# Optimization experiments

Measured on AMD Instinct MI355X. Metric: run time of the kernel, lower is better.

Reference implementation:

```python
import jax, jax.numpy as jnp
import numpy as np

H = 2048          # hidden size
NH = 32           # query heads
NKV = 8           # kv heads
HD = H // NH      # head dim = 64
GROUPS = NH // NKV
S = 2048          # seq len
B = 1
SCALE = HD ** -0.5


def _rope_tables(seq, dim, base=10000.0):
    inv = 1.0 / (base ** (np.arange(0, dim, 2, dtype=np.float32) / dim))
    t = np.arange(seq, dtype=np.float32)
    freqs = np.outer(t, inv)                     # [S, dim/2]
    emb = np.concatenate([freqs, freqs], axis=-1)  # [S, dim]
    return jnp.asarray(np.cos(emb)), jnp.asarray(np.sin(emb))


def setup_inputs() -> dict:
    key = jax.random.key(0)
    ks = jax.random.split(key, 5)
    x = jax.random.normal(ks[0], (B, S, H), dtype=jnp.float32)
    wq = jax.random.normal(ks[1], (H, NH * HD), dtype=jnp.float32) * (H ** -0.5)
    wk = jax.random.normal(ks[2], (H, NKV * HD), dtype=jnp.float32) * (H ** -0.5)
    wv = jax.random.normal(ks[3], (H, NKV * HD), dtype=jnp.float32) * (H ** -0.5)
    wo = jax.random.normal(ks[4], (NH * HD, H), dtype=jnp.float32) * (H ** -0.5)
    cos, sin = _rope_tables(S, HD)
    mask = jnp.tril(jnp.ones((S, S), dtype=bool))[None, None]  # causal [1,1,S,S]
    return {"x": x, "wq": wq, "wk": wk, "wv": wv, "wo": wo,
            "cos": cos, "sin": sin, "mask": mask}


def _rotate_half(t):
    t1, t2 = jnp.split(t, 2, axis=-1)
    return jnp.concatenate([-t2, t1], axis=-1)


def reference(x, wq, wk, wv, wo, cos, sin, mask):
    b, s, _ = x.shape
    # projections
    q = (x @ wq).reshape(b, s, NH, HD).transpose(0, 2, 1, 3)    # [B,NH,S,HD]
    k = (x @ wk).reshape(b, s, NKV, HD).transpose(0, 2, 1, 3)   # [B,NKV,S,HD]
    v = (x @ wv).reshape(b, s, NKV, HD).transpose(0, 2, 1, 3)
    # RoPE (cos/sin broadcast over batch and heads)
    c = cos[None, None]; sn = sin[None, None]
    q = q * c + _rotate_half(q) * sn
    k = k * c + _rotate_half(k) * sn
    # GQA: repeat kv heads to match query heads
    k = jnp.repeat(k, GROUPS, axis=1)                           # [B,NH,S,HD]
    v = jnp.repeat(v, GROUPS, axis=1)
    # scores + causal mask + softmax (dropout p=0 -> identity in eval)
    scores = SCALE * jnp.einsum('bhqd,bhkd->bhqk', q, k)
    scores = jnp.where(mask, scores, -jnp.inf)
    attn = jax.nn.softmax(scores, axis=-1)
    out = jnp.einsum('bhqk,bhkd->bhqd', attn, v)
    out = out.transpose(0, 2, 1, 3).reshape(b, s, NH * HD)
    return out @ wo
```

## Files before the change

### kernel.cpp

```cpp
#include <hip/hip_runtime.h>

typedef unsigned short u16;
typedef unsigned u32;
typedef u16 u16x8 __attribute__((ext_vector_type(8)));
typedef u16 u16x4 __attribute__((ext_vector_type(4)));
typedef u32 u32x4 __attribute__((ext_vector_type(4)));
typedef __bf16 bf8 __attribute__((ext_vector_type(8)));
typedef float f32x4 __attribute__((ext_vector_type(4)));
typedef float f32x16 __attribute__((ext_vector_type(16)));

__device__ __forceinline__ u16 f2b(float f) {
  unsigned u = __float_as_uint(f);
  u += 0x7FFFu + ((u >> 16) & 1u);
  return (u16)(u >> 16);
}
__device__ __forceinline__ float b2f(u16 h) {
  return __uint_as_float(((unsigned)h) << 16);
}
__device__ __forceinline__ bf8 asbf8(u16x8 v) {
  return __builtin_bit_cast(bf8, v);
}
__device__ __forceinline__ void gll16(const u16* g, u16* l) {
  __builtin_amdgcn_global_load_lds(
      (const __attribute__((address_space(1))) unsigned*)(g),
      (__attribute__((address_space(3))) unsigned*)(l), 16, 0, 0);
}
__device__ __forceinline__ u32 cvtpk(float lo, float hi) {
  u32 r;
  asm("v_cvt_pk_bf16_f32 %0, %1, %2" : "=v"(r) : "v"(lo), "v"(hi));
  return r;
}
__device__ __forceinline__ void plswap(u32& a, u32& b) {
  asm("v_permlane32_swap_b32 %0, %1" : "+v"(a), "+v"(b));
}
__device__ __forceinline__ float ex2(float x) {
  return __builtin_amdgcn_exp2f(x);
}
#define MFMA32(A,B,C) __builtin_amdgcn_mfma_f32_32x32x16_bf16(A,B,C,0,0,0)


__global__ __launch_bounds__(256) void xconv(const float* __restrict__ x,
                                             u16* __restrict__ xb) {
  int i = (blockIdx.x * 256 + threadIdx.x) * 4;
  float4 v = *(const float4*)(x + i);
  u16x4 o;
  o[0] = f2b(v.x); o[1] = f2b(v.y); o[2] = f2b(v.z); o[3] = f2b(v.w);
  *(u16x4*)(xb + i) = o;
}

__global__ __launch_bounds__(256) void wtrans(const float* __restrict__ in,
                                              u16* __restrict__ out,
                                              int N, int K) {
  __shared__ float tile[32][33];
  int tx = threadIdx.x & 31, ty = threadIdx.x >> 5;
  int n0 = blockIdx.x * 32, k0 = blockIdx.y * 32;
#pragma unroll
  for (int yy = 0; yy < 32; yy += 8)
    tile[ty + yy][tx] = in[(size_t)(k0 + ty + yy) * N + n0 + tx];
  __syncthreads();
#pragma unroll
  for (int yy = 0; yy < 32; yy += 8)
    out[(size_t)(n0 + ty + yy) * K + k0 + tx] = f2b(tile[tx][ty + yy]);
}

__global__ __launch_bounds__(256) void reduce_qkv(u16* __restrict__ p0,
                                                  const u16* __restrict__ p1,
                                                  const float* __restrict__ cs,
                                                  const float* __restrict__ sn) {
  int idx = blockIdx.x * 256 + threadIdx.x;
  int s = idx / 384, c8 = (idx % 384) * 8;
  size_t base = (size_t)s * 3072 + c8;
  if (c8 < 2560) {
    int hc = c8 & 63;
    if (hc >= 32) return;
    u16x8 a0 = *(const u16x8*)(p0 + base);
    u16x8 a1 = *(const u16x8*)(p1 + base);
    u16x8 b0 = *(const u16x8*)(p0 + base + 32);
    u16x8 b1 = *(const u16x8*)(p1 + base + 32);
    u16x8 oa, ob;
#pragma unroll
    for (int e = 0; e < 8; ++e) {
      float va = b2f(a0[e]) + b2f(a1[e]);
      float vb = b2f(b0[e]) + b2f(b1[e]);
      float c1 = cs[s * 64 + hc + e],      s1 = sn[s * 64 + hc + e];
      float c2 = cs[s * 64 + hc + 32 + e], s2 = sn[s * 64 + hc + 32 + e];
      oa[e] = f2b(va * c1 - vb * s1);
      ob[e] = f2b(vb * c2 + va * s2);
    }
    *(u16x8*)(p0 + base)      = oa;
    *(u16x8*)(p0 + base + 32) = ob;
  } else {
    u16x8 a0 = *(const u16x8*)(p0 + base);
    u16x8 a1 = *(const u16x8*)(p1 + base);
    u16x8 o;
#pragma unroll
    for (int e = 0; e < 8; ++e) o[e] = f2b(b2f(a0[e]) + b2f(a1[e]));
    *(u16x8*)(p0 + base) = o;
  }
}

__global__ __launch_bounds__(256) void reduce_out(const u16* __restrict__ p0,
                                                  const u16* __restrict__ p1,
                                                  float* __restrict__ out) {
  int idx = blockIdx.x * 256 + threadIdx.x;
  size_t base = (size_t)idx * 8;
  u16x8 a0 = *(const u16x8*)(p0 + base);
  u16x8 a1 = *(const u16x8*)(p1 + base);
  float4 lo, hi;
  lo.x = b2f(a0[0]) + b2f(a1[0]); lo.y = b2f(a0[1]) + b2f(a1[1]);
  lo.z = b2f(a0[2]) + b2f(a1[2]); lo.w = b2f(a0[3]) + b2f(a1[3]);
  hi.x = b2f(a0[4]) + b2f(a1[4]); hi.y = b2f(a0[5]) + b2f(a1[5]);
  hi.z = b2f(a0[6]) + b2f(a1[6]); hi.w = b2f(a0[7]) + b2f(a1[7]);
  *(float4*)(out + base)     = lo;
  *(float4*)(out + base + 4) = hi;
}

__global__ __launch_bounds__(256) void kvtrans_f(const u16* __restrict__ qkv,
                                                 u16* __restrict__ Kf,
                                                 u16* __restrict__ Vf) {
  int bid = blockIdx.x;
  if (bid < 512) {
    int tid = bid * 256 + threadIdx.x;
    int s = tid >> 6, cc = tid & 63;
    int kh = cc >> 3, c = cc & 7;
    int j = c >> 1, hi = c & 1;
    int b = s >> 5, la = s & 31;
    u16x8 v = *(const u16x8*)(qkv + (size_t)s * 3072 + 2048 + cc * 8);
    *(u16x8*)(Kf + ((((size_t)(kh * 64 + b) * 4 + j) * 2 + hi) * 32 + la) * 8) = v;
  } else {
    int tid = (bid - 512) * 256 + threadIdx.x;
    int s = tid >> 6, cc = tid & 63;
    int kh = cc >> 3, c = cc & 7;
    int m = c >> 2, laB = (c & 3) * 8;
    int b = s >> 5, s5 = s & 31;
    int jj = s5 >> 4, hi = (s5 >> 3) & 1, e = s5 & 7;
    u16x8 v = *(const u16x8*)(qkv + (size_t)s * 3072 + 2560 + cc * 8);
    u16* dst = Vf + (((size_t)(kh * 64 + b) * 4 + m * 2 + jj) * 64 + hi * 32 + laB) * 8 + e;
#pragma unroll
    for (int i = 0; i < 8; ++i) dst[i * 8] = v[i];
  }
}


__global__ __launch_bounds__(256) void gemm_sk(const u16* __restrict__ A,
                                               const u16* __restrict__ Bt,
                                               u16* __restrict__ C0,
                                               u16* __restrict__ C1,
                                               int N, int Kfull, int KH) {
  __shared__ __align__(16) u16 As[128 * 64];
  __shared__ __align__(16) u16 Bs[128 * 64];
  const int t = threadIdx.x;
  const int lane = t & 63, wid = t >> 6;
  const int wm = (wid >> 1) * 64, wn = (wid & 1) * 64;
  const int la = lane & 15, lg = lane >> 4;
  const int m0 = blockIdx.y * 128, n0 = blockIdx.x * 128;
  const int kbeg = blockIdx.z * KH;
  u16* C = blockIdx.z ? C1 : C0;

  const int srow0 = wid * 32 + (lane >> 3);
  const int scolsw = (((lane & 7) ^ (lane >> 3))) * 8;
  const u16* Ap = A + (size_t)(m0 + srow0) * Kfull + kbeg + scolsw;
  const u16* Bp = Bt + (size_t)(n0 + srow0) * Kfull + kbeg + scolsw;
  u16* Adst = &As[wid * 2048];
  u16* Bdst = &Bs[wid * 2048];
  const size_t rstep8 = (size_t)8 * Kfull;

  f32x4 acc[4][4] = {};

  for (int k0 = 0; k0 < KH; k0 += 64) {
    __syncthreads();
#pragma unroll
    for (int cc = 0; cc < 4; ++cc)
      gll16(Ap + k0 + cc * rstep8, Adst + cc * 512);
#pragma unroll
    for (int cc = 0; cc < 4; ++cc)
      gll16(Bp + k0 + cc * rstep8, Bdst + cc * 512);
    __syncthreads();
#pragma unroll
    for (int kk = 0; kk < 2; ++kk) {
      bf8 af[4], bfr[4];
#pragma unroll
      for (int i = 0; i < 4; ++i) {
        const int row = wm + i * 16 + la;
        const int c8 = (kk * 4 + lg) ^ (row & 7);
        af[i] = asbf8(*(const u16x8*)(&As[row * 64 + c8 * 8]));
      }
#pragma unroll
      for (int j = 0; j < 4; ++j) {
        const int row = wn + j * 16 + la;
        const int c8 = (kk * 4 + lg) ^ (row & 7);
        bfr[j] = asbf8(*(const u16x8*)(&Bs[row * 64 + c8 * 8]));
      }
      __builtin_amdgcn_s_setprio(1);
#pragma unroll
      for (int i = 0; i < 4; ++i)
#pragma unroll
        for (int j = 0; j < 4; ++j)
          acc[i][j] = __builtin_amdgcn_mfma_f32_16x16x32_bf16(af[i], bfr[j],
                                                              acc[i][j], 0, 0, 0);
      __builtin_amdgcn_s_setprio(0);
    }
  }

#pragma unroll
  for (int i = 0; i < 4; ++i)
#pragma unroll
    for (int j = 0; j < 4; ++j)
#pragma unroll
      for (int r = 0; r < 4; ++r) {
        int row = m0 + wm + i * 16 + lg * 4 + r;
        int col = n0 + wn + j * 16 + la;
        C[(size_t)row * N + col] = f2b(acc[i][j][r]);
      }
}


#define STEPL(buf, bb) do {                                          \
    const u16* p_ = &smem[(((h2) << 1) | (buf)) * 4096 + lane8];     \
    bf8 K0 = asbf8(*(const u16x8*)(p_));                             \
    bf8 K1 = asbf8(*(const u16x8*)(p_ + 512));                       \
    bf8 K2 = asbf8(*(const u16x8*)(p_ + 1024));                      \
    bf8 K3 = asbf8(*(const u16x8*)(p_ + 1536));                      \
    bf8 V0 = asbf8(*(const u16x8*)(p_ + 2048));                      \
    bf8 V1 = asbf8(*(const u16x8*)(p_ + 2560));                      \
    bf8 V2 = asbf8(*(const u16x8*)(p_ + 3072));                      \
    bf8 V3 = asbf8(*(const u16x8*)(p_ + 3584));                      \
    f32x16 s = {};                                                   \
    __builtin_amdgcn_s_setprio(1);                                   \
    s = MFMA32(K0, qf0, s);                                          \
    s = MFMA32(K1, qf1, s);                                          \
    s = MFMA32(K2, qf2, s);                                          \
    s = MFMA32(K3, qf3, s);                                          \
    __builtin_amdgcn_s_setprio(0);                                   \
    if ((bb) == kmax) {                                              \
      _Pragma("unroll") for (int r = 0; r < 16; ++r) {               \
        int kvr = (bb) * 32 + (r & 3) + 8 * (r >> 2) + 4 * hi;       \
        if (kvr > q0w + la) s[r] = -1e30f;                           \
      }                                                              \
    }                                                                \
    _Pragma("unroll") for (int r = 0; r < 16; ++r)                   \
      s[r] = ex2(s[r] - 32.0f);                                      \
    float z0 = s[0] + s[1],   z1 = s[2] + s[3];                      \
    float z2 = s[4] + s[5],   z3 = s[6] + s[7];                      \
    float z4 = s[8] + s[9],   z5 = s[10] + s[11];                    \
    float z6 = s[12] + s[13], z7 = s[14] + s[15];                    \
    l_run += ((z0 + z1) + (z2 + z3)) + ((z4 + z5) + (z6 + z7));      \
    u32 c0 = cvtpk(s[0], s[1]),   c1 = cvtpk(s[2], s[3]);            \
    u32 c2 = cvtpk(s[4], s[5]),   c3 = cvtpk(s[6], s[7]);            \
    u32 c4 = cvtpk(s[8], s[9]),   c5 = cvtpk(s[10], s[11]);          \
    u32 c6 = cvtpk(s[12], s[13]), c7 = cvtpk(s[14], s[15]);          \
    plswap(c0, c2); plswap(c1, c3); plswap(c4, c6); plswap(c5, c7);  \
    u32x4 t0; t0[0] = c0; t0[1] = c1; t0[2] = c2; t0[3] = c3;        \
    u32x4 t1; t1[0] = c4; t1[1] = c5; t1[2] = c6; t1[3] = c7;        \
    bf8 pa0 = __builtin_bit_cast(bf8, t0);                           \
    bf8 pa1 = __builtin_bit_cast(bf8, t1);                           \
    __builtin_amdgcn_s_setprio(1);                                   \
    o0 = MFMA32(pa0, V0, o0);                                        \
    o0 = MFMA32(pa1, V1, o0);                                        \
    o1 = MFMA32(pa0, V2, o1);                                        \
    o1 = MFMA32(pa1, V3, o1);                                        \
    __builtin_amdgcn_s_setprio(0);                                   \
  } while (0)

#define STG(bb, buf) do {                                            \
    u16* d_ = &smem[((((h2) << 1) | (buf)) * 4096) + wq * 1024];     \
    const u16* kp_ = Kg + (size_t)(bb) * 2048 + wq * 1024 + lane8;   \
    const u16* vp_ = Vg + (size_t)(bb) * 2048 + wq * 1024 + lane8;   \
    gll16(kp_, d_);                                                  \
    gll16(kp_ + 512, d_ + 512);                                      \
    gll16(vp_, d_ + 2048);                                           \
    gll16(vp_ + 512, d_ + 2560);                                     \
  } while (0)

__global__ __launch_bounds__(256, 4) void attn_fwd(const u16* __restrict__ qkv,
                                                   const u16* __restrict__ Kf,
                                                   const u16* __restrict__ Vf,
                                                   u16* __restrict__ aout) {
  const int head = blockIdx.x;
  const int qt = 31 - (int)blockIdx.y;
  const int Q0 = qt * 64;
  const int Kb = qt * 2;
  const int nb = Kb + 2;
  const int ha = nb >> 1;
  const int kh = head >> 2;
  const int t = threadIdx.x;
  const int w = t >> 6, lane = t & 63;
  const int h2 = w >> 1;
  const int wq = w & 1;
  const int la = lane & 31;
  const int hi = lane >> 5;
  const int lane8 = lane * 8;
  const int q0w = Q0 + 32 * wq;
  const int kmax = Kb + wq;

  __shared__ __align__(16) u16 smem[16384];
  __shared__ float lM[4][32];

  bf8 qf0, qf1, qf2, qf3;
  {
    const u16* qp = qkv + (size_t)(q0w + la) * 3072 + head * 64 + hi * 8;
    const float SC = 0.125f * 1.44269504088896340736f;
#define QLOAD(dst, kk) do {                                          \
      u16x8 v = *(const u16x8*)(qp + (kk) * 16);                     \
      u16x8 sv;                                                      \
      _Pragma("unroll") for (int e = 0; e < 8; ++e)                  \
        sv[e] = f2b(b2f(v[e]) * SC);                                 \
      dst = asbf8(sv);                                               \
    } while (0)
    QLOAD(qf0, 0); QLOAD(qf1, 1); QLOAD(qf2, 2); QLOAD(qf3, 3);
#undef QLOAD
  }

  const u16* Kg = Kf + (size_t)kh * 131072;
  const u16* Vg = Vf + (size_t)kh * 131072;

  f32x16 o0 = {}, o1 = {};
  float l_run = 0.f;

  STG(h2 ? ha : 0, 0);
  __syncthreads();

  for (int i = 0; i < ha; ++i) {
    if (i + 1 < ha) STG(h2 ? (ha + i + 1) : (i + 1), (i + 1) & 1);
    const int bb = h2 ? (ha + i) : i;
    if (bb <= kmax) STEPL(i & 1, bb);
    __syncthreads();
  }

  {
    float lt = l_run + __shfl_xor(l_run, 32);
    if (lane < 32) lM[w][lane] = lt;
#pragma unroll
    for (int r = 0; r < 16; ++r) {
      int crow = (r & 3) + 8 * (r >> 2) + 4 * hi;
      smem[(w * 32 + crow) * 72 + la]      = f2b(o0[r]);
      smem[(w * 32 + crow) * 72 + la + 32] = f2b(o1[r]);
    }
  }
  __syncthreads();

#pragma unroll
  for (int it = 0; it < 2; ++it) {
    const int id = t + it * 256;
    const int q = id >> 3, d0 = (id & 7) * 8;
    const int wA = q >> 5, crow = q & 31;
    float inv = 1.0f / (lM[wA][crow] + lM[wA + 2][crow]);
    u16x8 a = *(const u16x8*)&smem[((wA)     * 32 + crow) * 72 + d0];
    u16x8 b = *(const u16x8*)&smem[((wA + 2) * 32 + crow) * 72 + d0];
    u16x8 outv;
#pragma unroll
    for (int j = 0; j < 8; ++j)
      outv[j] = f2b((b2f(a[j]) + b2f(b[j])) * inv);
    *(u16x8*)(aout + (size_t)(Q0 + q) * 2048 + head * 64 + d0) = outv;
  }
}


extern "C" void kernel_launch(void* const* d_in, const int* in_sizes, int n_in,
                              void* d_out, int out_size, void* d_ws, size_t ws_size,
                              hipStream_t stream) {
  (void)in_sizes; (void)n_in; (void)out_size; (void)ws_size;
  const float* x  = (const float*)d_in[0];
  const float* wq = (const float*)d_in[1];
  const float* wk = (const float*)d_in[2];
  const float* wv = (const float*)d_in[3];
  const float* wo = (const float*)d_in[4];
  const float* cs = (const float*)d_in[5];
  const float* sn = (const float*)d_in[6];

  u16* ws    = (u16*)d_ws;
  u16* xb    = ws;
  u16* wqkvT = ws + 4194304;
  u16* qkv   = ws + 10485760;
  u16* woT   = ws + 16777216;
  u16* ext   = ws + 20971520;
  u16* Kf    = wqkvT;
  u16* Vf    = wqkvT + 1048576;
  u16* aout  = xb;
  u16* op0   = qkv;
  u16* op1   = ext;

  xconv<<<4096, 256, 0, stream>>>(x, xb);
  wtrans<<<dim3(64, 64), 256, 0, stream>>>(wq, wqkvT, 2048, 2048);
  wtrans<<<dim3(16, 64), 256, 0, stream>>>(wk, wqkvT + (size_t)2048 * 2048, 512, 2048);
  wtrans<<<dim3(16, 64), 256, 0, stream>>>(wv, wqkvT + (size_t)2560 * 2048, 512, 2048);
  wtrans<<<dim3(64, 64), 256, 0, stream>>>(wo, woT, 2048, 2048);

  gemm_sk<<<dim3(24, 16, 2), 256, 0, stream>>>(xb, wqkvT, qkv, ext, 3072, 2048, 1024);
  reduce_qkv<<<3072, 256, 0, stream>>>(qkv, ext, cs, sn);
  kvtrans_f<<<1024, 256, 0, stream>>>(qkv, Kf, Vf);
  attn_fwd<<<dim3(32, 32), 256, 0, stream>>>(qkv, Kf, Vf, aout);
  gemm_sk<<<dim3(16, 16, 2), 256, 0, stream>>>(aout, woT, op0, op1, 2048, 2048, 1024);
  reduce_out<<<2048, 256, 0, stream>>>(op0, op1, (float*)d_out);
}
```

Measured before the change: 140.5 us.

## Fuse KV layout transform into reduce kernel and stage 64-key blocks in attention

The split-K reduction kernel now writes the RoPE'd K and the summed V straight into the fragment layouts the attention kernel consumes, so the separate kvtrans_f launch and its extra pass over K/V are gone. The attention kernel now stages 64-key blocks (two 32-key groups) per iteration with doubled shared memory, halving the number of barriers and loop steps. The larger LDS footprint lowers the occupancy hint from 4 to 2 blocks per CU, which risks less latency hiding. The V path now does scattered 2-byte stores from the reduce kernel.

```diff
diff --git a/kernel.cpp b/kernel.cpp
--- a/kernel.cpp
+++ b/kernel.cpp
@@ -65,6 +65,8 @@
 
 __global__ __launch_bounds__(256) void reduce_qkv(u16* __restrict__ p0,
                                                   const u16* __restrict__ p1,
+                                                  u16* __restrict__ Kf,
+                                                  u16* __restrict__ Vf,
                                                   const float* __restrict__ cs,
                                                   const float* __restrict__ sn) {
   int idx = blockIdx.x * 256 + threadIdx.x;
@@ -87,15 +89,31 @@
       oa[e] = f2b(va * c1 - vb * s1);
       ob[e] = f2b(vb * c2 + va * s2);
     }
-    *(u16x8*)(p0 + base)      = oa;
-    *(u16x8*)(p0 + base + 32) = ob;
+    if (c8 < 2048) {
+      *(u16x8*)(p0 + base)      = oa;
+      *(u16x8*)(p0 + base + 32) = ob;
+    } else {
+      int kh = (c8 - 2048) >> 6;
+      int d0 = hc;
+      int b = s >> 5, la = s & 31;
+      int j0 = d0 >> 4, hi0 = (d0 >> 3) & 1;
+      size_t f0 = ((((size_t)(kh * 64 + b) * 4 + j0) * 2 + hi0) * 32 + la) * 8;
+      size_t f1 = ((((size_t)(kh * 64 + b) * 4 + j0 + 2) * 2 + hi0) * 32 + la) * 8;
+      *(u16x8*)(Kf + f0) = oa;
+      *(u16x8*)(Kf + f1) = ob;
+    }
   } else {
     u16x8 a0 = *(const u16x8*)(p0 + base);
     u16x8 a1 = *(const u16x8*)(p1 + base);
-    u16x8 o;
-#pragma unroll
-    for (int e = 0; e < 8; ++e) o[e] = f2b(b2f(a0[e]) + b2f(a1[e]));
-    *(u16x8*)(p0 + base) = o;
+    int c = c8 - 2560;
+    int kh = c >> 6, d0 = c & 63;
+    int m = d0 >> 5, la0 = d0 & 31;
+    int b = s >> 5, s5 = s & 31;
+    int jj = s5 >> 4, hi = (s5 >> 3) & 1, e = s5 & 7;
+    u16* dst = Vf + (((size_t)(kh * 64 + b) * 4 + m * 2 + jj) * 64 + hi * 32 + la0) * 8 + e;
+#pragma unroll
+    for (int i = 0; i < 8; ++i)
+      dst[i * 8] = f2b(b2f(a0[i]) + b2f(a1[i]));
   }
 }
 
@@ -115,32 +133,6 @@
   *(float4*)(out + base + 4) = hi;
 }
 
-__global__ __launch_bounds__(256) void kvtrans_f(const u16* __restrict__ qkv,
-                                                 u16* __restrict__ Kf,
-                                                 u16* __restrict__ Vf) {
-  int bid = blockIdx.x;
-  if (bid < 512) {
-    int tid = bid * 256 + threadIdx.x;
-    int s = tid >> 6, cc = tid & 63;
-    int kh = cc >> 3, c = cc & 7;
-    int j = c >> 1, hi = c & 1;
-    int b = s >> 5, la = s & 31;
-    u16x8 v = *(const u16x8*)(qkv + (size_t)s * 3072 + 2048 + cc * 8);
-    *(u16x8*)(Kf + ((((size_t)(kh * 64 + b) * 4 + j) * 2 + hi) * 32 + la) * 8) = v;
-  } else {
-    int tid = (bid - 512) * 256 + threadIdx.x;
-    int s = tid >> 6, cc = tid & 63;
-    int kh = cc >> 3, c = cc & 7;
-    int m = c >> 2, laB = (c & 3) * 8;
-    int b = s >> 5, s5 = s & 31;
-    int jj = s5 >> 4, hi = (s5 >> 3) & 1, e = s5 & 7;
-    u16x8 v = *(const u16x8*)(qkv + (size_t)s * 3072 + 2560 + cc * 8);
-    u16* dst = Vf + (((size_t)(kh * 64 + b) * 4 + m * 2 + jj) * 64 + hi * 32 + laB) * 8 + e;
-#pragma unroll
-    for (int i = 0; i < 8; ++i) dst[i * 8] = v[i];
-  }
-}
-
 
 __global__ __launch_bounds__(256) void gemm_sk(const u16* __restrict__ A,
                                                const u16* __restrict__ Bt,
@@ -215,73 +207,87 @@
 }
 
 
+#define GROUPG(g, bb, base_) do {                                    \
+    const int kvb_ = (bb) * 64 + (g) * 32;                           \
+    if (kvb_ <= q0w + 31) {                                          \
+      const u16* pk_ = (base_) + (g) * 2048;                         \
+      const u16* pv_ = (base_) + 4096 + (g) * 2048;                  \
+      bf8 K0 = asbf8(*(const u16x8*)(pk_));                          \
+      bf8 K1 = asbf8(*(const u16x8*)(pk_ + 512));                    \
+      bf8 K2 = asbf8(*(const u16x8*)(pk_ + 1024));                   \
+      bf8 K3 = asbf8(*(const u16x8*)(pk_ + 1536));                   \
+      bf8 V0 = asbf8(*(const u16x8*)(pv_));                          \
+      bf8 V1 = asbf8(*(const u16x8*)(pv_ + 512));                    \
+      bf8 V2 = asbf8(*(const u16x8*)(pv_ + 1024));                   \
+      bf8 V3 = asbf8(*(const u16x8*)(pv_ + 1536));                   \
+      f32x16 s = {};                                                 \
+      __builtin_amdgcn_s_setprio(1);                                 \
+      s = MFMA32(K0, qf0, s);                                        \
+      s = MFMA32(K1, qf1, s);                                        \
+      s = MFMA32(K2, qf2, s);                                        \
+      s = MFMA32(K3, qf3, s);                                        \
+      __builtin_amdgcn_s_setprio(0);                                 \
+      if ((bb) == nb64 - 1) {                                        \
+        _Pragma("unroll") for (int r = 0; r < 16; ++r) {             \
+          int kvr = kvb_ + (r & 3) + 8 * (r >> 2) + 4 * hi;          \
+          if (kvr > q0w + la) s[r] = -1e30f;                         \
+        }                                                            \
+      }                                                              \
+      _Pragma("unroll") for (int r = 0; r < 16; ++r)                 \
+        s[r] = ex2(s[r] - 32.0f);                                    \
+      float z0 = s[0] + s[1],   z1 = s[2] + s[3];                    \
+      float z2 = s[4] + s[5],   z3 = s[6] + s[7];                    \
+      float z4 = s[8] + s[9],   z5 = s[10] + s[11];                  \
+      float z6 = s[12] + s[13], z7 = s[14] + s[15];                  \
+      l_run += ((z0 + z1) + (z2 + z3)) + ((z4 + z5) + (z6 + z7));    \
+      u32 c0 = cvtpk(s[0], s[1]),   c1 = cvtpk(s[2], s[3]);          \
+      u32 c2 = cvtpk(s[4], s[5]),   c3 = cvtpk(s[6], s[7]);          \
+      u32 c4 = cvtpk(s[8], s[9]),   c5 = cvtpk(s[10], s[11]);        \
+      u32 c6 = cvtpk(s[12], s[13]), c7 = cvtpk(s[14], s[15]);        \
+      plswap(c0, c2); plswap(c1, c3); plswap(c4, c6); plswap(c5, c7);\
+      u32x4 t0; t0[0] = c0; t0[1] = c1; t0[2] = c2; t0[3] = c3;      \
+      u32x4 t1; t1[0] = c4; t1[1] = c5; t1[2] = c6; t1[3] = c7;      \
+      bf8 pa0 = __builtin_bit_cast(bf8, t0);                         \
+      bf8 pa1 = __builtin_bit_cast(bf8, t1);                         \
+      __builtin_amdgcn_s_setprio(1);                                 \
+      o0 = MFMA32(pa0, V0, o0);                                      \
+      o0 = MFMA32(pa1, V1, o0);                                      \
+      o1 = MFMA32(pa0, V2, o1);                                      \
+      o1 = MFMA32(pa1, V3, o1);                                      \
+      __builtin_amdgcn_s_setprio(0);                                 \
+    }                                                                \
+  } while (0)
+
 #define STEPL(buf, bb) do {                                          \
-    const u16* p_ = &smem[(((h2) << 1) | (buf)) * 4096 + lane8];     \
-    bf8 K0 = asbf8(*(const u16x8*)(p_));                             \
-    bf8 K1 = asbf8(*(const u16x8*)(p_ + 512));                       \
-    bf8 K2 = asbf8(*(const u16x8*)(p_ + 1024));                      \
-    bf8 K3 = asbf8(*(const u16x8*)(p_ + 1536));                      \
-    bf8 V0 = asbf8(*(const u16x8*)(p_ + 2048));                      \
-    bf8 V1 = asbf8(*(const u16x8*)(p_ + 2560));                      \
-    bf8 V2 = asbf8(*(const u16x8*)(p_ + 3072));                      \
-    bf8 V3 = asbf8(*(const u16x8*)(p_ + 3584));                      \
-    f32x16 s = {};                                                   \
-    __builtin_amdgcn_s_setprio(1);                                   \
-    s = MFMA32(K0, qf0, s);                                          \
-    s = MFMA32(K1, qf1, s);                                          \
-    s = MFMA32(K2, qf2, s);                                          \
-    s = MFMA32(K3, qf3, s);                                          \
-    __builtin_amdgcn_s_setprio(0);                                   \
-    if ((bb) == kmax) {                                              \
-      _Pragma("unroll") for (int r = 0; r < 16; ++r) {               \
-        int kvr = (bb) * 32 + (r & 3) + 8 * (r >> 2) + 4 * hi;       \
-        if (kvr > q0w + la) s[r] = -1e30f;                           \
-      }                                                              \
-    }                                                                \
-    _Pragma("unroll") for (int r = 0; r < 16; ++r)                   \
-      s[r] = ex2(s[r] - 32.0f);                                      \
-    float z0 = s[0] + s[1],   z1 = s[2] + s[3];                      \
-    float z2 = s[4] + s[5],   z3 = s[6] + s[7];                      \
-    float z4 = s[8] + s[9],   z5 = s[10] + s[11];                    \
-    float z6 = s[12] + s[13], z7 = s[14] + s[15];                    \
-    l_run += ((z0 + z1) + (z2 + z3)) + ((z4 + z5) + (z6 + z7));      \
-    u32 c0 = cvtpk(s[0], s[1]),   c1 = cvtpk(s[2], s[3]);            \
-    u32 c2 = cvtpk(s[4], s[5]),   c3 = cvtpk(s[6], s[7]);            \
-    u32 c4 = cvtpk(s[8], s[9]),   c5 = cvtpk(s[10], s[11]);          \
-    u32 c6 = cvtpk(s[12], s[13]), c7 = cvtpk(s[14], s[15]);          \
-    plswap(c0, c2); plswap(c1, c3); plswap(c4, c6); plswap(c5, c7);  \
-    u32x4 t0; t0[0] = c0; t0[1] = c1; t0[2] = c2; t0[3] = c3;        \
-    u32x4 t1; t1[0] = c4; t1[1] = c5; t1[2] = c6; t1[3] = c7;        \
-    bf8 pa0 = __builtin_bit_cast(bf8, t0);                           \
-    bf8 pa1 = __builtin_bit_cast(bf8, t1);                           \
-    __builtin_amdgcn_s_setprio(1);                                   \
-    o0 = MFMA32(pa0, V0, o0);                                        \
-    o0 = MFMA32(pa1, V1, o0);                                        \
-    o1 = MFMA32(pa0, V2, o1);                                        \
-    o1 = MFMA32(pa1, V3, o1);                                        \
-    __builtin_amdgcn_s_setprio(0);                                   \
+    const u16* base_ = &smem[((((h2) << 1) | (buf)) * 8192) + lane8];\
+    GROUPG(0, bb, base_);                                            \
+    GROUPG(1, bb, base_);                                            \
   } while (0)
 
 #define STG(bb, buf) do {                                            \
-    u16* d_ = &smem[((((h2) << 1) | (buf)) * 4096) + wq * 1024];     \
-    const u16* kp_ = Kg + (size_t)(bb) * 2048 + wq * 1024 + lane8;   \
-    const u16* vp_ = Vg + (size_t)(bb) * 2048 + wq * 1024 + lane8;   \
+    u16* d_ = &smem[((((h2) << 1) | (buf)) * 8192) + wq * 2048];     \
+    const u16* kp_ = Kg + (size_t)(bb) * 4096 + wq * 2048 + lane8;   \
+    const u16* vp_ = Vg + (size_t)(bb) * 4096 + wq * 2048 + lane8;   \
     gll16(kp_, d_);                                                  \
     gll16(kp_ + 512, d_ + 512);                                      \
-    gll16(vp_, d_ + 2048);                                           \
-    gll16(vp_ + 512, d_ + 2560);                                     \
+    gll16(kp_ + 1024, d_ + 1024);                                    \
+    gll16(kp_ + 1536, d_ + 1536);                                    \
+    gll16(vp_, d_ + 4096);                                           \
+    gll16(vp_ + 512, d_ + 4608);                                     \
+    gll16(vp_ + 1024, d_ + 5120);                                    \
+    gll16(vp_ + 1536, d_ + 5632);                                    \
   } while (0)
 
-__global__ __launch_bounds__(256, 4) void attn_fwd(const u16* __restrict__ qkv,
+__global__ __launch_bounds__(256, 2) void attn_fwd(const u16* __restrict__ qkv,
                                                    const u16* __restrict__ Kf,
                                                    const u16* __restrict__ Vf,
                                                    u16* __restrict__ aout) {
   const int head = blockIdx.x;
   const int qt = 31 - (int)blockIdx.y;
   const int Q0 = qt * 64;
-  const int Kb = qt * 2;
-  const int nb = Kb + 2;
-  const int ha = nb >> 1;
+  const int nb64 = qt + 1;
+  const int haA = (nb64 + 1) >> 1;
+  const int haB = nb64 >> 1;
   const int kh = head >> 2;
   const int t = threadIdx.x;
   const int w = t >> 6, lane = t & 63;
@@ -291,9 +297,10 @@
   const int hi = lane >> 5;
   const int lane8 = lane * 8;
   const int q0w = Q0 + 32 * wq;
-  const int kmax = Kb + wq;
-
-  __shared__ __align__(16) u16 smem[16384];
+  const int myn = h2 ? haB : haA;
+  const int mybase = h2 ? haA : 0;
+
+  __shared__ __align__(16) u16 smem[32768];
   __shared__ float lM[4][32];
 
   bf8 qf0, qf1, qf2, qf3;
@@ -317,13 +324,12 @@
   f32x16 o0 = {}, o1 = {};
   float l_run = 0.f;
 
-  STG(h2 ? ha : 0, 0);
+  if (myn > 0) STG(mybase, 0);
   __syncthreads();
 
-  for (int i = 0; i < ha; ++i) {
-    if (i + 1 < ha) STG(h2 ? (ha + i + 1) : (i + 1), (i + 1) & 1);
-    const int bb = h2 ? (ha + i) : i;
-    if (bb <= kmax) STEPL(i & 1, bb);
+  for (int i = 0; i < haA; ++i) {
+    if (i + 1 < myn) STG(mybase + i + 1, (i + 1) & 1);
+    if (i < myn) STEPL(i & 1, mybase + i);
     __syncthreads();
   }
 
@@ -387,8 +393,7 @@
   wtrans<<<dim3(64, 64), 256, 0, stream>>>(wo, woT, 2048, 2048);
 
   gemm_sk<<<dim3(24, 16, 2), 256, 0, stream>>>(xb, wqkvT, qkv, ext, 3072, 2048, 1024);
-  reduce_qkv<<<3072, 256, 0, stream>>>(qkv, ext, cs, sn);
-  kvtrans_f<<<1024, 256, 0, stream>>>(qkv, Kf, Vf);
+  reduce_qkv<<<3072, 256, 0, stream>>>(qkv, ext, Kf, Vf, cs, sn);
   attn_fwd<<<dim3(32, 32), 256, 0, stream>>>(qkv, Kf, Vf, aout);
   gemm_sk<<<dim3(16, 16, 2), 256, 0, stream>>>(aout, woT, op0, op1, 2048, 2048, 1024);
   reduce_out<<<2048, 256, 0, stream>>>(op0, op1, (float*)d_out);
```

Result: no change. 138.0 us (-1.8%).
